# Performance work log

Measured on AMD Instinct MI355X. Metric: run time of the kernel, lower is better.

The kernel has to match this reference:

```python
import jax, jax.numpy as jnp
import numpy as np

P = 1_000_000          # num node-pair paths (sum of n_i^2 over batch)
D = 5                  # max_path_distance
E = 64                 # edge_embedding_dim (== hidden_dim of x)
NUM_EDGES = 500_000
NUM_NODES = 30_000


def setup_inputs() -> dict:
    key = jax.random.key(0)
    k1, k2, k3, k4, k5 = jax.random.split(key, 5)
    x = jax.random.normal(k1, (NUM_NODES, E), dtype=jnp.float32)
    edge_embedding = jax.random.normal(k2, (NUM_EDGES, E), dtype=jnp.float32)
    # paths padded with -1 beyond each path's length (length in [0, D])
    raw = jax.random.randint(k3, (P, D), 0, NUM_EDGES)
    lengths = jax.random.randint(k4, (P,), 0, D + 1)
    edge_paths = jnp.where(jnp.arange(D)[None, :] < lengths[:, None], raw, -1)
    edge_vector = jax.random.normal(k5, (D, E), dtype=jnp.float32)  # nn.Parameter
    return {"x": x, "edge_embedding": edge_embedding,
            "edge_paths": edge_paths, "edge_vector": edge_vector}


def reference(x, edge_embedding, edge_paths, edge_vector):
    # mask of valid hops along each path
    edge_mask = edge_paths != -1                      # (P, D) bool
    path_lengths = edge_mask.sum(axis=-1)             # (P,) int
    safe_idx = jnp.where(edge_mask, edge_paths, 0)    # (P, D)
    # Original math: sum_d sum_e emb[path[p,d], e] * edge_vector[d, e] over valid d.
    # Fused form: precompute per-(edge, position) dot products, then gather scalars
    # instead of materializing the (P, D, E) tensor.
    scores = edge_embedding @ edge_vector.T           # (NUM_EDGES, D)
    gathered = scores[safe_idx, jnp.arange(D)[None, :]]  # (P, D)
    enc = jnp.sum(gathered * edge_mask, axis=-1)      # (P,)
    # divide by path length only where path is non-empty
    denom = jnp.maximum(path_lengths, 1).astype(enc.dtype)
    enc = jnp.where(path_lengths != 0, enc / denom, enc)
    return enc
```

## Files before the change

### kernel.cpp

```cpp
#include <hip/hip_runtime.h>

#define NE 500000
#define NP 1000000
#define DD 5
#define EE 64

typedef float f32x4 __attribute__((ext_vector_type(4)));
typedef _Float16 f16;

__global__ void scores_kernel(const float* __restrict__ emb,
                              const float* __restrict__ ev,
                              f16* __restrict__ scores_t) {
    int e = blockIdx.x * blockDim.x + threadIdx.x;
    if (e >= NE) return;

    const f32x4* row = reinterpret_cast<const f32x4*>(emb + (size_t)e * EE);
    f32x4 r[16];
#pragma unroll
    for (int it = 0; it < 16; ++it) r[it] = row[it];

#pragma unroll
    for (int d = 0; d < DD; ++d) {
        const f32x4* w4 = reinterpret_cast<const f32x4*>(ev + (size_t)d * EE);
        float acc = 0.f;
#pragma unroll
        for (int it = 0; it < 16; ++it) {
            const f32x4 w = w4[it];
            acc += r[it].x * w.x + r[it].y * w.y + r[it].z * w.z + r[it].w * w.w;
        }
        scores_t[(size_t)d * NE + e] = (f16)acc;
    }
}

__global__ void gather_kernel(const int* __restrict__ paths,
                              const f16* __restrict__ scores_t,
                              float* __restrict__ out) {
    int p = blockIdx.x * blockDim.x + threadIdx.x;
    if (p >= NP) return;

    int ix[DD];
#pragma unroll
    for (int d = 0; d < DD; ++d)
        ix[d] = __builtin_nontemporal_load(paths + (size_t)p * DD + d);

    float v0 = 0.f, v1 = 0.f, v2 = 0.f, v3 = 0.f, v4 = 0.f;
    if (ix[0] >= 0) v0 = (float)scores_t[(size_t)0 * NE + ix[0]];
    if (ix[1] >= 0) v1 = (float)scores_t[(size_t)1 * NE + ix[1]];
    if (ix[2] >= 0) v2 = (float)scores_t[(size_t)2 * NE + ix[2]];
    if (ix[3] >= 0) v3 = (float)scores_t[(size_t)3 * NE + ix[3]];
    if (ix[4] >= 0) v4 = (float)scores_t[(size_t)4 * NE + ix[4]];

    int cnt = (ix[0] >= 0) + (ix[1] >= 0) + (ix[2] >= 0) + (ix[3] >= 0) + (ix[4] >= 0);
    float acc = (v0 + v1) + (v2 + v3) + v4;
    float r = (cnt > 0) ? acc / (float)cnt : 0.f;
    __builtin_nontemporal_store(r, out + p);
}

extern "C" void kernel_launch(void* const* d_in, const int* in_sizes, int n_in,
                              void* d_out, int out_size, void* d_ws, size_t ws_size,
                              hipStream_t stream) {
    const float* emb   = (const float*)d_in[1];
    const int*   paths = (const int*)d_in[2];
    const float* ev    = (const float*)d_in[3];
    float*       out   = (float*)d_out;

    f16* scores_t = (f16*)d_ws;

    {
        const int block = 256;
        const int grid = (NE + block - 1) / block;
        scores_kernel<<<grid, block, 0, stream>>>(emb, ev, scores_t);
    }
    {
        const int block = 256;
        const int grid = (NP + block - 1) / block;
        gather_kernel<<<grid, block, 0, stream>>>(paths, scores_t, out);
    }
}
```

Baseline: 49.43 us.

## Split each embedding row across four lanes with DPP butterfly reduction

The scores kernel now assigns four threads per embedding row. Each thread loads interleaved 16-byte chunks, so neighbouring lanes read contiguous memory and loads coalesce. Partial dot products are combined with DPP quad butterfly adds, and each lane writes one of the five scores. Row loads are nontemporal. This targets the strided per-thread 256-byte row reads of the old layout, at the cost of four times as many threads and some extra reduction instructions.

```diff
diff --git a/kernel.cpp b/kernel.cpp
--- a/kernel.cpp
+++ b/kernel.cpp
@@ -8,28 +8,55 @@
 typedef float f32x4 __attribute__((ext_vector_type(4)));
 typedef _Float16 f16;
 
-__global__ void scores_kernel(const float* __restrict__ emb,
-                              const float* __restrict__ ev,
-                              f16* __restrict__ scores_t) {
-    int e = blockIdx.x * blockDim.x + threadIdx.x;
-    if (e >= NE) return;
+__device__ __forceinline__ float quad_bfly_add(float x) {
+    int a = __builtin_amdgcn_mov_dpp(__float_as_int(x), 0xB1, 0xf, 0xf, true);
+    x += __int_as_float(a);
+    int b = __builtin_amdgcn_mov_dpp(__float_as_int(x), 0x4E, 0xf, 0xf, true);
+    x += __int_as_float(b);
+    return x;
+}
 
-    const f32x4* row = reinterpret_cast<const f32x4*>(emb + (size_t)e * EE);
-    f32x4 r[16];
+__global__ void __launch_bounds__(256)
+scores_kernel(const float* __restrict__ emb,
+              const float* __restrict__ ev,
+              f16* __restrict__ scores_t) {
+    const int t   = blockIdx.x * blockDim.x + threadIdx.x;
+    const int row = t >> 2;
+    const int q   = t & 3;
+    if (row >= NE) return;
+
+    float a0 = 0.f, a1 = 0.f, a2 = 0.f, a3 = 0.f, a4 = 0.f;
+    const float* rowp = emb + (size_t)row * EE + q * 4;
+    const float* evp  = ev + q * 4;
 #pragma unroll
-    for (int it = 0; it < 16; ++it) r[it] = row[it];
+    for (int it = 0; it < 4; ++it) {
+        const f32x4 r = __builtin_nontemporal_load(
+            reinterpret_cast<const f32x4*>(rowp + it * 16));
+        f32x4 w;
+        w = *reinterpret_cast<const f32x4*>(evp + 0 * EE + it * 16);
+        a0 += r.x * w.x + r.y * w.y + r.z * w.z + r.w * w.w;
+        w = *reinterpret_cast<const f32x4*>(evp + 1 * EE + it * 16);
+        a1 += r.x * w.x + r.y * w.y + r.z * w.z + r.w * w.w;
+        w = *reinterpret_cast<const f32x4*>(evp + 2 * EE + it * 16);
+        a2 += r.x * w.x + r.y * w.y + r.z * w.z + r.w * w.w;
+        w = *reinterpret_cast<const f32x4*>(evp + 3 * EE + it * 16);
+        a3 += r.x * w.x + r.y * w.y + r.z * w.z + r.w * w.w;
+        w = *reinterpret_cast<const f32x4*>(evp + 4 * EE + it * 16);
+        a4 += r.x * w.x + r.y * w.y + r.z * w.z + r.w * w.w;
+    }
 
-#pragma unroll
-    for (int d = 0; d < DD; ++d) {
-        const f32x4* w4 = reinterpret_cast<const f32x4*>(ev + (size_t)d * EE);
-        float acc = 0.f;
-#pragma unroll
-        for (int it = 0; it < 16; ++it) {
-            const f32x4 w = w4[it];
-            acc += r[it].x * w.x + r[it].y * w.y + r[it].z * w.z + r[it].w * w.w;
-        }
-        scores_t[(size_t)d * NE + e] = (f16)acc;
-    }
+    a0 = quad_bfly_add(a0);
+    a1 = quad_bfly_add(a1);
+    a2 = quad_bfly_add(a2);
+    a3 = quad_bfly_add(a3);
+    a4 = quad_bfly_add(a4);
+
+    float mine = a0;
+    mine = (q == 1) ? a1 : mine;
+    mine = (q == 2) ? a2 : mine;
+    mine = (q == 3) ? a3 : mine;
+    scores_t[(size_t)q * NE + row] = (f16)mine;
+    if (q == 0) scores_t[(size_t)4 * NE + row] = (f16)a4;
 }
 
 __global__ void gather_kernel(const int* __restrict__ paths,
@@ -67,8 +94,9 @@
     f16* scores_t = (f16*)d_ws;
 
     {
+        const long long total = (long long)NE * 4;
         const int block = 256;
-        const int grid = (NE + block - 1) / block;
+        const int grid = (int)((total + block - 1) / block);
         scores_kernel<<<grid, block, 0, stream>>>(emb, ev, scores_t);
     }
     {
```

Measured after the change: 62.06 us. 1.26x slower.
